# Performance work log

Hardware: AMD Instinct MI355X
Metric: run time of the kernel (lower is better)

Reference implementation:

```python
import jax, jax.numpy as jnp
import numpy as np


def setup_inputs() -> dict:
    key = jax.random.key(0)
    k1, k2, k3, k4 = jax.random.split(key, 4)
    B, T, N, D = 4, 8, 512, 256
    BT = B * T
    x = jax.random.normal(k1, (BT, N, D), dtype=jnp.float32)
    A_causal = jax.random.uniform(k2, (B, N, N), dtype=jnp.float32)
    W_qkv = jax.random.normal(k3, (3 * D, D), dtype=jnp.float32) * (D ** -0.5)
    W_proj = jax.random.normal(k4, (D, D), dtype=jnp.float32) * (D ** -0.5)
    b_proj = jnp.zeros((D,), dtype=jnp.float32)
    causal_lambda = jnp.ones((1,), dtype=jnp.float32) * 0.1
    return {
        "x": x,
        "A_causal": A_causal,
        "W_qkv": W_qkv,
        "W_proj": W_proj,
        "b_proj": b_proj,
        "causal_lambda": causal_lambda,
        "num_frames": 8,
    }


def reference(x, A_causal, W_qkv, W_proj, b_proj, causal_lambda, num_frames):
    BT, N, D = x.shape
    H = 8
    hd = D // H
    scale = hd ** -0.5
    # qkv projection (torch Linear: x @ W.T), split into q,k,v of shape [BT,H,N,hd]
    qkv = (x @ W_qkv.T).reshape(BT, N, 3, H, hd)
    qkv = jnp.transpose(qkv, (2, 0, 3, 1, 4))  # [3,BT,H,N,hd]
    q, k, v = qkv[0], qkv[1], qkv[2]
    attn = jnp.einsum("bhnd,bhmd->bhnm", q, k) * scale  # [BT,H,N,N]
    # expand A_causal [B,N,N] over frames (axis 0) and heads (broadcast axis 1)
    A_exp = jnp.repeat(A_causal, num_frames, axis=0)[:, None, :, :]  # [BT,1,N,N]
    attn = attn + causal_lambda[0] * A_exp
    attn = jax.nn.softmax(attn, axis=-1)
    out = jnp.einsum("bhnm,bhmd->bhnd", attn, v)  # [BT,H,N,hd]
    out = jnp.transpose(out, (0, 2, 1, 3)).reshape(BT, N, D)
    return out @ W_proj.T + b_proj
```

## Files before the change

### kernel.cpp

```cpp
#include <hip/hip_runtime.h>
#include <hip/hip_bf16.h>

typedef unsigned short u16;
typedef unsigned int   u32;
typedef __attribute__((ext_vector_type(8))) short short8;
typedef __attribute__((ext_vector_type(4))) float f32x4;

static __device__ __forceinline__ u16 f2b(float f) {
    __hip_bfloat16 h = __float2bfloat16(f);
    return *reinterpret_cast<u16*>(&h);
}
static __device__ __forceinline__ u32 pk2(float a, float b) {
    return (u32)f2b(a) | ((u32)f2b(b) << 16);
}

#define LDK 72

__global__ __launch_bounds__(256) void prep_A(const float* __restrict__ A,
                                              const float* __restrict__ LAM,
                                              u16* __restrict__ AB) {
    const float lam = LAM[0];
    const int i = (blockIdx.x * 256 + threadIdx.x) * 8;
    const float4 a = *(const float4*)(A + i);
    const float4 b = *(const float4*)(A + i + 4);
    uint4 o;
    o.x = pk2(lam * a.x, lam * a.y);
    o.y = pk2(lam * a.z, lam * a.w);
    o.z = pk2(lam * b.x, lam * b.y);
    o.w = pk2(lam * b.z, lam * b.w);
    *(uint4*)(AB + i) = o;
}

__global__ __launch_bounds__(256) void qkv_gemm(const float* __restrict__ X,
                                                const float* __restrict__ W,
                                                u16* __restrict__ qo,
                                                u16* __restrict__ ko,
                                                u16* __restrict__ vt) {
    __shared__ u16 SH[2 * 128 * LDK];
    u16* Xs = SH;
    u16* Ws = SH + 128 * LDK;
    const int t    = threadIdx.x;
    const int m0   = blockIdx.x << 7;
    const int o0   = blockIdx.y << 7;
    const int lane = t & 63;
    const int wid  = t >> 6;
    const int wr   = (wid >> 1) << 6;
    const int wc   = (wid & 1) << 6;
    const int ln   = lane & 15;
    const int quad = lane >> 4;

    const int r  = t >> 1;
    const int hf = (t & 1) << 5;
    const float* xg = X + (size_t)(m0 + r) * 256 + hf;
    const float* wg = W + (size_t)(o0 + r) * 256 + hf;
    uint4* xls = (uint4*)&Xs[r * LDK + hf];
    uint4* wls = (uint4*)&Ws[r * LDK + hf];

    f32x4 acc[4][4] = {};

    for (int kc = 0; kc < 256; kc += 64) {
        const float4* xp = (const float4*)(xg + kc);
        const float4* wp = (const float4*)(wg + kc);
        float xv[32], wv[32];
#pragma unroll
        for (int i = 0; i < 8; ++i) {
            float4 a = xp[i]; xv[4*i] = a.x; xv[4*i+1] = a.y; xv[4*i+2] = a.z; xv[4*i+3] = a.w;
            float4 b = wp[i]; wv[4*i] = b.x; wv[4*i+1] = b.y; wv[4*i+2] = b.z; wv[4*i+3] = b.w;
        }
        uint4 xq[4], wq[4];
#pragma unroll
        for (int i = 0; i < 4; ++i) {
            xq[i].x = pk2(xv[8*i],   xv[8*i+1]); xq[i].y = pk2(xv[8*i+2], xv[8*i+3]);
            xq[i].z = pk2(xv[8*i+4], xv[8*i+5]); xq[i].w = pk2(xv[8*i+6], xv[8*i+7]);
            wq[i].x = pk2(wv[8*i],   wv[8*i+1]); wq[i].y = pk2(wv[8*i+2], wv[8*i+3]);
            wq[i].z = pk2(wv[8*i+4], wv[8*i+5]); wq[i].w = pk2(wv[8*i+6], wv[8*i+7]);
        }
        __syncthreads();
#pragma unroll
        for (int i = 0; i < 4; ++i) { xls[i] = xq[i]; wls[i] = wq[i]; }
        __syncthreads();
#pragma unroll
        for (int kk = 0; kk < 64; kk += 32) {
            short8 a[4], b[4];
#pragma unroll
            for (int i = 0; i < 4; ++i)
                a[i] = *(const short8*)&Xs[(wr + i * 16 + ln) * LDK + kk + quad * 8];
#pragma unroll
            for (int j = 0; j < 4; ++j)
                b[j] = *(const short8*)&Ws[(wc + j * 16 + ln) * LDK + kk + quad * 8];
#pragma unroll
            for (int i = 0; i < 4; ++i)
#pragma unroll
                for (int j = 0; j < 4; ++j)
                    acc[i][j] = __builtin_amdgcn_mfma_f32_16x16x32_bf16(a[i], b[j], acc[i][j], 0, 0, 0);
        }
    }

    const int which = o0 >> 8;
    if (which < 2) {
        const float qscale = (which == 0) ? 0.17677669529663689f : 1.0f;
        u16* dst = (which == 0) ? qo : ko;
#pragma unroll
        for (int i = 0; i < 4; ++i) {
            const int mb = m0 + wr + i * 16 + quad * 4;
#pragma unroll
            for (int j = 0; j < 4; ++j) {
                const int o   = o0 + wc + j * 16 + ln;
                const int rem = o & 255;
                const int hh  = rem >> 5;
                const int dd  = rem & 31;
#pragma unroll
                for (int rr = 0; rr < 4; ++rr) {
                    const int m  = mb + rr;
                    const int bt = m >> 9;
                    const int n  = m & 511;
                    dst[(((size_t)bt * 8 + hh) * 512 + n) * 32 + dd] = f2b(acc[i][j][rr] * qscale);
                }
            }
        }
    } else {
        __syncthreads();
        u16* T = SH;
#pragma unroll
        for (int i = 0; i < 4; ++i) {
            const int ml = wr + i * 16 + quad * 4;
#pragma unroll
            for (int j = 0; j < 4; ++j) {
                const int ol = wc + j * 16 + ln;
                uint2 pv;
                pv.x = pk2(acc[i][j][0], acc[i][j][1]);
                pv.y = pk2(acc[i][j][2], acc[i][j][3]);
                *(uint2*)&T[ol * 136 + ml] = pv;
            }
        }
        __syncthreads();
        const int row = t >> 1;
        const int seg = (t & 1) << 6;
        const int o   = o0 + row;
        const int rem = o & 255;
        const int hh  = rem >> 5;
        const int dd  = rem & 31;
        const int bt  = m0 >> 9;
        u16* dstv = vt + (((size_t)bt * 8 + hh) * 32 + dd) * 512 + (m0 & 511) + seg;
#pragma unroll
        for (int kk2 = 0; kk2 < 8; ++kk2) {
            uint4 val = *(const uint4*)&T[row * 136 + seg + kk2 * 8];
            *(uint4*)(dstv + kk2 * 8) = val;
        }
    }
}

__global__ __launch_bounds__(256, 3) void attn_mfma(const u16* __restrict__ Q,
                                                    const u16* __restrict__ K,
                                                    const u16* __restrict__ VT,
                                                    const u16* __restrict__ AB,
                                                    const int* __restrict__ NF,
                                                    u16* __restrict__ AO) {
    __shared__ u16 Ks[2][128 * 40];
    __shared__ u16 Vs[2][32 * 136];
    __shared__ u16 Ps[4][32 * 40];
    const int t    = threadIdx.x;
    const int w    = t >> 6;
    const int lane = t & 63;
    const int ln   = lane & 15;
    const int quad = lane >> 4;
    const int L    = blockIdx.x;
    const int g    = (L & 7) + (((L >> 3) & 1) << 3);
    const int j    = L >> 4;
    const int qt   = g & 3;
    const int h    = j & 7;
    const int bt   = (g >> 2) * 8 + (j >> 3);
    const int bh   = bt * 8 + h;
    const int q0   = qt * 128 + w * 32;
    const size_t base = (size_t)bh * (512 * 32);
    const int b    = bt / NF[0];
    const u16* Ab  = AB + (size_t)b * 512 * 512;
    const u16* Ar0 = Ab + (size_t)(q0 + ln) * 512 + quad * 4;
    const u16* Ar1 = Ab + (size_t)(q0 + 16 + ln) * 512 + quad * 4;

    const int krow = t >> 2, kcol = (t & 3) * 8;
    const int vd   = t >> 4, vn   = (t & 15) * 8;
    const u16* Kg = K + base;
    const u16* Vg = VT + base;

    {
        uint4 s0 = *(const uint4*)(Kg + (size_t)krow * 32 + kcol);
        uint4 s1 = *(const uint4*)(Kg + (size_t)(64 + krow) * 32 + kcol);
        uint4 s2 = *(const uint4*)(Vg + (size_t)vd * 512 + vn);
        uint4 s3 = *(const uint4*)(Vg + (size_t)(16 + vd) * 512 + vn);
        *(uint4*)&Ks[0][krow * 40 + kcol]        = s0;
        *(uint4*)&Ks[0][(64 + krow) * 40 + kcol] = s1;
        *(uint4*)&Vs[0][vd * 136 + vn]           = s2;
        *(uint4*)&Vs[0][(16 + vd) * 136 + vn]    = s3;
    }

    short8 qf[2];
#pragma unroll
    for (int nt = 0; nt < 2; ++nt)
        qf[nt] = *(const short8*)(Q + base + (size_t)(q0 + nt * 16 + ln) * 32 + quad * 8);

    f32x4 o[2][2] = {};
    float lsum0 = 0.f, lsum1 = 0.f;
    __syncthreads();

    int cur = 0;
    for (int jt = 0; jt < 512; jt += 128) {
        const int nxt = cur ^ 1;
        const bool more = jt < 384;
        uint4 t0 = {}, t1 = {}, t2 = {}, t3 = {};
        if (more) {
            t0 = *(const uint4*)(Kg + (size_t)(jt + 128 + krow) * 32 + kcol);
            t1 = *(const uint4*)(Kg + (size_t)(jt + 192 + krow) * 32 + kcol);
            t2 = *(const uint4*)(Vg + (size_t)vd * 512 + jt + 128 + vn);
            t3 = *(const uint4*)(Vg + (size_t)(16 + vd) * 512 + jt + 128 + vn);
        }
        uint2 ar[16];
#pragma unroll
        for (int mt = 0; mt < 8; ++mt) {
            ar[2*mt]     = *(const uint2*)(Ar0 + jt + mt * 16);
            ar[2*mt + 1] = *(const uint2*)(Ar1 + jt + mt * 16);
        }

        float ps0 = 0.f, ps1 = 0.f;
#pragma unroll
        for (int ks = 0; ks < 4; ++ks) {
#pragma unroll
            for (int mm = 0; mm < 2; ++mm) {
                const int mt = 2 * ks + mm;
                short8 ka = *(const short8*)&Ks[cur][(mt * 16 + ln) * 40 + quad * 8];
                f32x4 c0, c1;
                c0[0] = __uint_as_float(ar[2*mt].x << 16);   c0[1] = __uint_as_float(ar[2*mt].x & 0xffff0000u);
                c0[2] = __uint_as_float(ar[2*mt].y << 16);   c0[3] = __uint_as_float(ar[2*mt].y & 0xffff0000u);
                c1[0] = __uint_as_float(ar[2*mt+1].x << 16); c1[1] = __uint_as_float(ar[2*mt+1].x & 0xffff0000u);
                c1[2] = __uint_as_float(ar[2*mt+1].y << 16); c1[3] = __uint_as_float(ar[2*mt+1].y & 0xffff0000u);
                const f32x4 s0 = __builtin_amdgcn_mfma_f32_16x16x32_bf16(ka, qf[0], c0, 0, 0, 0);
                const f32x4 s1 = __builtin_amdgcn_mfma_f32_16x16x32_bf16(ka, qf[1], c1, 0, 0, 0);
                const float p00 = __expf(s0[0]), p01 = __expf(s0[1]), p02 = __expf(s0[2]), p03 = __expf(s0[3]);
                const float p10 = __expf(s1[0]), p11 = __expf(s1[1]), p12 = __expf(s1[2]), p13 = __expf(s1[3]);
                ps0 += (p00 + p01) + (p02 + p03);
                ps1 += (p10 + p11) + (p12 + p13);
                uint2 w0; w0.x = pk2(p00, p01); w0.y = pk2(p02, p03);
                uint2 w1; w1.x = pk2(p10, p11); w1.y = pk2(p12, p13);
                *(uint2*)&Ps[w][ln * 40 + mm * 16 + quad * 4]        = w0;
                *(uint2*)&Ps[w][(16 + ln) * 40 + mm * 16 + quad * 4] = w1;
            }
            short8 pa0 = *(const short8*)&Ps[w][ln * 40 + quad * 8];
            short8 pa1 = *(const short8*)&Ps[w][(16 + ln) * 40 + quad * 8];
            short8 vb0 = *(const short8*)&Vs[cur][ln * 136 + ks * 32 + quad * 8];
            short8 vb1 = *(const short8*)&Vs[cur][(16 + ln) * 136 + ks * 32 + quad * 8];
            o[0][0] = __builtin_amdgcn_mfma_f32_16x16x32_bf16(pa0, vb0, o[0][0], 0, 0, 0);
            o[0][1] = __builtin_amdgcn_mfma_f32_16x16x32_bf16(pa0, vb1, o[0][1], 0, 0, 0);
            o[1][0] = __builtin_amdgcn_mfma_f32_16x16x32_bf16(pa1, vb0, o[1][0], 0, 0, 0);
            o[1][1] = __builtin_amdgcn_mfma_f32_16x16x32_bf16(pa1, vb1, o[1][1], 0, 0, 0);
        }

        if (more) {
            *(uint4*)&Ks[nxt][krow * 40 + kcol]        = t0;
            *(uint4*)&Ks[nxt][(64 + krow) * 40 + kcol] = t1;
            *(uint4*)&Vs[nxt][vd * 136 + vn]           = t2;
            *(uint4*)&Vs[nxt][(16 + vd) * 136 + vn]    = t3;
        }
        ps0 += __shfl_xor(ps0, 16); ps0 += __shfl_xor(ps0, 32); lsum0 += ps0;
        ps1 += __shfl_xor(ps1, 16); ps1 += __shfl_xor(ps1, 32); lsum1 += ps1;
        __syncthreads();
        cur = nxt;
    }

#pragma unroll
    for (int r = 0; r < 4; ++r) {
        const int src = quad * 4 + r;
        const float i0 = 1.f / __shfl(lsum0, src);
        const float i1 = 1.f / __shfl(lsum1, src);
        const int n0 = qt * 128 + w * 32 + quad * 4 + r;
#pragma unroll
        for (int ntd = 0; ntd < 2; ++ntd) {
            AO[((size_t)bt * 512 + n0) * 256 + h * 32 + ntd * 16 + ln]      = f2b(o[0][ntd][r] * i0);
            AO[((size_t)bt * 512 + n0 + 16) * 256 + h * 32 + ntd * 16 + ln] = f2b(o[1][ntd][r] * i1);
        }
    }
}

__global__ __launch_bounds__(256) void proj_gemm(const u16* __restrict__ X,
                                                 const float* __restrict__ W,
                                                 const float* __restrict__ BIAS,
                                                 float* __restrict__ OUT) {
    __shared__ u16 Xs[128 * LDK];
    __shared__ u16 Ws[128 * LDK];
    const int t    = threadIdx.x;
    const int m0   = blockIdx.x << 7;
    const int o0   = blockIdx.y << 7;
    const int lane = t & 63;
    const int wid  = t >> 6;
    const int wr   = (wid >> 1) << 6;
    const int wc   = (wid & 1) << 6;
    const int ln   = lane & 15;
    const int quad = lane >> 4;

    const int r  = t >> 1;
    const int hf = (t & 1) << 5;
    const u16*   xg = X + (size_t)(m0 + r) * 256 + hf;
    const float* wg = W + (size_t)(o0 + r) * 256 + hf;
    uint4* xls = (uint4*)&Xs[r * LDK + hf];
    uint4* wls = (uint4*)&Ws[r * LDK + hf];

    f32x4 acc[4][4] = {};

    for (int kc = 0; kc < 256; kc += 64) {
        const uint4*  xp = (const uint4*)(xg + kc);
        const float4* wp = (const float4*)(wg + kc);
        uint4 x0 = xp[0], x1 = xp[1], x2 = xp[2], x3 = xp[3];
        float wv[32];
#pragma unroll
        for (int i = 0; i < 8; ++i) {
            float4 b = wp[i]; wv[4*i] = b.x; wv[4*i+1] = b.y; wv[4*i+2] = b.z; wv[4*i+3] = b.w;
        }
        uint4 wq[4];
#pragma unroll
        for (int i = 0; i < 4; ++i) {
            wq[i].x = pk2(wv[8*i],   wv[8*i+1]); wq[i].y = pk2(wv[8*i+2], wv[8*i+3]);
            wq[i].z = pk2(wv[8*i+4], wv[8*i+5]); wq[i].w = pk2(wv[8*i+6], wv[8*i+7]);
        }
        __syncthreads();
        xls[0] = x0; xls[1] = x1; xls[2] = x2; xls[3] = x3;
#pragma unroll
        for (int i = 0; i < 4; ++i) wls[i] = wq[i];
        __syncthreads();
#pragma unroll
        for (int kk = 0; kk < 64; kk += 32) {
            short8 a[4], b[4];
#pragma unroll
            for (int i = 0; i < 4; ++i)
                a[i] = *(const short8*)&Xs[(wr + i * 16 + ln) * LDK + kk + quad * 8];
#pragma unroll
            for (int j = 0; j < 4; ++j)
                b[j] = *(const short8*)&Ws[(wc + j * 16 + ln) * LDK + kk + quad * 8];
#pragma unroll
            for (int i = 0; i < 4; ++i)
#pragma unroll
                for (int j = 0; j < 4; ++j)
                    acc[i][j] = __builtin_amdgcn_mfma_f32_16x16x32_bf16(a[i], b[j], acc[i][j], 0, 0, 0);
        }
    }

#pragma unroll
    for (int i = 0; i < 4; ++i) {
        const int mb = m0 + wr + i * 16 + quad * 4;
#pragma unroll
        for (int j = 0; j < 4; ++j) {
            const int o  = o0 + wc + j * 16 + ln;
            const float bo = BIAS[o];
#pragma unroll
            for (int rr = 0; rr < 4; ++rr) {
                const int m = mb + rr;
                OUT[(size_t)m * 256 + o] = acc[i][j][rr] + bo;
            }
        }
    }
}

extern "C" void kernel_launch(void* const* d_in, const int* in_sizes, int n_in,
                              void* d_out, int out_size, void* d_ws, size_t ws_size,
                              hipStream_t stream) {
    (void)in_sizes; (void)n_in; (void)out_size; (void)ws_size;
    const float* x     = (const float*)d_in[0];
    const float* A     = (const float*)d_in[1];
    const float* Wqkv  = (const float*)d_in[2];
    const float* Wproj = (const float*)d_in[3];
    const float* bproj = (const float*)d_in[4];
    const float* lam   = (const float*)d_in[5];
    const int*   nf    = (const int*)d_in[6];
    float* out = (float*)d_out;

    u16* q  = (u16*)d_ws;
    u16* k  = q + 4194304;
    u16* vt = k + 4194304;
    u16* ao = vt + 4194304;
    u16* AB = ao + 4194304;

    prep_A  <<<dim3(512), 256, 0, stream>>>(A, lam, AB);
    qkv_gemm<<<dim3(128, 6), 256, 0, stream>>>(x, Wqkv, q, k, vt);
    attn_mfma<<<dim3(1024), 256, 0, stream>>>(q, k, vt, AB, nf, ao);
    proj_gemm<<<dim3(128, 2), 256, 0, stream>>>(ao, Wproj, bproj, out);
}
```

Measured before the change: 168.1 us.

## Pre-convert weights to bf16 in prep kernel and prefetch bias tiles in attention

The prep kernel now also converts W_qkv and W_proj to bf16 once. Both GEMMs then load bf16 weights directly instead of reading fp32 and converting in every block. The attention loop prefetches the next bias tile into registers one iteration ahead and drops the conditional on the last K/V prefetch by wrapping the index. This costs extra registers and one redundant tile load at the end of each attention block.

Result: faster. 161.4 us (-4.0%).

```diff
diff --git a/kernel.cpp b/kernel.cpp
--- a/kernel.cpp
+++ b/kernel.cpp
@@ -16,23 +16,34 @@
 
 #define LDK 72
 
-__global__ __launch_bounds__(256) void prep_A(const float* __restrict__ A,
-                                              const float* __restrict__ LAM,
-                                              u16* __restrict__ AB) {
-    const float lam = LAM[0];
-    const int i = (blockIdx.x * 256 + threadIdx.x) * 8;
-    const float4 a = *(const float4*)(A + i);
-    const float4 b = *(const float4*)(A + i + 4);
+__global__ __launch_bounds__(256) void prep(const float* __restrict__ A,
+                                            const float* __restrict__ LAM,
+                                            const float* __restrict__ Wq,
+                                            const float* __restrict__ Wp,
+                                            u16* __restrict__ AB,
+                                            u16* __restrict__ wqb,
+                                            u16* __restrict__ wpb) {
+    const int bid = blockIdx.x;
+    const float* src;
+    u16* dst;
+    float scale;
+    int base;
+    if (bid < 512)      { src = A;  dst = AB;  scale = LAM[0]; base = bid * 2048; }
+    else if (bid < 608) { src = Wq; dst = wqb; scale = 1.0f;   base = (bid - 512) * 2048; }
+    else                { src = Wp; dst = wpb; scale = 1.0f;   base = (bid - 608) * 2048; }
+    const int i = base + threadIdx.x * 8;
+    const float4 a = *(const float4*)(src + i);
+    const float4 b = *(const float4*)(src + i + 4);
     uint4 o;
-    o.x = pk2(lam * a.x, lam * a.y);
-    o.y = pk2(lam * a.z, lam * a.w);
-    o.z = pk2(lam * b.x, lam * b.y);
-    o.w = pk2(lam * b.z, lam * b.w);
-    *(uint4*)(AB + i) = o;
+    o.x = pk2(scale * a.x, scale * a.y);
+    o.y = pk2(scale * a.z, scale * a.w);
+    o.z = pk2(scale * b.x, scale * b.y);
+    o.w = pk2(scale * b.z, scale * b.w);
+    *(uint4*)(dst + i) = o;
 }
 
 __global__ __launch_bounds__(256) void qkv_gemm(const float* __restrict__ X,
-                                                const float* __restrict__ W,
+                                                const u16* __restrict__ WB,
                                                 u16* __restrict__ qo,
                                                 u16* __restrict__ ko,
                                                 u16* __restrict__ vt) {
@@ -52,7 +63,7 @@
     const int r  = t >> 1;
     const int hf = (t & 1) << 5;
     const float* xg = X + (size_t)(m0 + r) * 256 + hf;
-    const float* wg = W + (size_t)(o0 + r) * 256 + hf;
+    const u16*   wg = WB + (size_t)(o0 + r) * 256 + hf;
     uint4* xls = (uint4*)&Xs[r * LDK + hf];
     uint4* wls = (uint4*)&Ws[r * LDK + hf];
 
@@ -60,24 +71,23 @@
 
     for (int kc = 0; kc < 256; kc += 64) {
         const float4* xp = (const float4*)(xg + kc);
-        const float4* wp = (const float4*)(wg + kc);
-        float xv[32], wv[32];
+        const uint4*  wp = (const uint4*)(wg + kc);
+        float xv[32];
 #pragma unroll
         for (int i = 0; i < 8; ++i) {
             float4 a = xp[i]; xv[4*i] = a.x; xv[4*i+1] = a.y; xv[4*i+2] = a.z; xv[4*i+3] = a.w;
-            float4 b = wp[i]; wv[4*i] = b.x; wv[4*i+1] = b.y; wv[4*i+2] = b.z; wv[4*i+3] = b.w;
-        }
-        uint4 xq[4], wq[4];
+        }
+        uint4 w0 = wp[0], w1 = wp[1], w2 = wp[2], w3 = wp[3];
+        uint4 xq[4];
 #pragma unroll
         for (int i = 0; i < 4; ++i) {
             xq[i].x = pk2(xv[8*i],   xv[8*i+1]); xq[i].y = pk2(xv[8*i+2], xv[8*i+3]);
             xq[i].z = pk2(xv[8*i+4], xv[8*i+5]); xq[i].w = pk2(xv[8*i+6], xv[8*i+7]);
-            wq[i].x = pk2(wv[8*i],   wv[8*i+1]); wq[i].y = pk2(wv[8*i+2], wv[8*i+3]);
-            wq[i].z = pk2(wv[8*i+4], wv[8*i+5]); wq[i].w = pk2(wv[8*i+6], wv[8*i+7]);
-        }
-        __syncthreads();
-#pragma unroll
-        for (int i = 0; i < 4; ++i) { xls[i] = xq[i]; wls[i] = wq[i]; }
+        }
+        __syncthreads();
+#pragma unroll
+        for (int i = 0; i < 4; ++i) xls[i] = xq[i];
+        wls[0] = w0; wls[1] = w1; wls[2] = w2; wls[3] = w3;
         __syncthreads();
 #pragma unroll
         for (int kk = 0; kk < 64; kk += 32) {
@@ -193,6 +203,12 @@
         *(uint4*)&Vs[0][vd * 136 + vn]           = s2;
         *(uint4*)&Vs[0][(16 + vd) * 136 + vn]    = s3;
     }
+    uint2 ar[16];
+#pragma unroll
+    for (int mt = 0; mt < 8; ++mt) {
+        ar[2*mt]     = *(const uint2*)(Ar0 + mt * 16);
+        ar[2*mt + 1] = *(const uint2*)(Ar1 + mt * 16);
+    }
 
     short8 qf[2];
 #pragma unroll
@@ -206,19 +222,16 @@
     int cur = 0;
     for (int jt = 0; jt < 512; jt += 128) {
         const int nxt = cur ^ 1;
-        const bool more = jt < 384;
-        uint4 t0 = {}, t1 = {}, t2 = {}, t3 = {};
-        if (more) {
-            t0 = *(const uint4*)(Kg + (size_t)(jt + 128 + krow) * 32 + kcol);
-            t1 = *(const uint4*)(Kg + (size_t)(jt + 192 + krow) * 32 + kcol);
-            t2 = *(const uint4*)(Vg + (size_t)vd * 512 + jt + 128 + vn);
-            t3 = *(const uint4*)(Vg + (size_t)(16 + vd) * 512 + jt + 128 + vn);
-        }
-        uint2 ar[16];
+        const int jn  = (jt + 128) & 511;
+        uint4 t0 = *(const uint4*)(Kg + (size_t)(jn + krow) * 32 + kcol);
+        uint4 t1 = *(const uint4*)(Kg + (size_t)(jn + 64 + krow) * 32 + kcol);
+        uint4 t2 = *(const uint4*)(Vg + (size_t)vd * 512 + jn + vn);
+        uint4 t3 = *(const uint4*)(Vg + (size_t)(16 + vd) * 512 + jn + vn);
+        uint2 arn[16];
 #pragma unroll
         for (int mt = 0; mt < 8; ++mt) {
-            ar[2*mt]     = *(const uint2*)(Ar0 + jt + mt * 16);
-            ar[2*mt + 1] = *(const uint2*)(Ar1 + jt + mt * 16);
+            arn[2*mt]     = *(const uint2*)(Ar0 + jn + mt * 16);
+            arn[2*mt + 1] = *(const uint2*)(Ar1 + jn + mt * 16);
         }
 
         float ps0 = 0.f, ps1 = 0.f;
@@ -254,15 +267,15 @@
             o[1][1] = __builtin_amdgcn_mfma_f32_16x16x32_bf16(pa1, vb1, o[1][1], 0, 0, 0);
         }
 
-        if (more) {
-            *(uint4*)&Ks[nxt][krow * 40 + kcol]        = t0;
-            *(uint4*)&Ks[nxt][(64 + krow) * 40 + kcol] = t1;
-            *(uint4*)&Vs[nxt][vd * 136 + vn]           = t2;
-            *(uint4*)&Vs[nxt][(16 + vd) * 136 + vn]    = t3;
-        }
+        *(uint4*)&Ks[nxt][krow * 40 + kcol]        = t0;
+        *(uint4*)&Ks[nxt][(64 + krow) * 40 + kcol] = t1;
+        *(uint4*)&Vs[nxt][vd * 136 + vn]           = t2;
+        *(uint4*)&Vs[nxt][(16 + vd) * 136 + vn]    = t3;
         ps0 += __shfl_xor(ps0, 16); ps0 += __shfl_xor(ps0, 32); lsum0 += ps0;
         ps1 += __shfl_xor(ps1, 16); ps1 += __shfl_xor(ps1, 32); lsum1 += ps1;
         __syncthreads();
+#pragma unroll
+        for (int i = 0; i < 16; ++i) ar[i] = arn[i];
         cur = nxt;
     }
 
@@ -281,7 +294,7 @@
 }
 
 __global__ __launch_bounds__(256) void proj_gemm(const u16* __restrict__ X,
-                                                 const float* __restrict__ W,
+                                                 const u16* __restrict__ WB,
                                                  const float* __restrict__ BIAS,
                                                  float* __restrict__ OUT) {
     __shared__ u16 Xs[128 * LDK];
@@ -298,32 +311,21 @@
 
     const int r  = t >> 1;
     const int hf = (t & 1) << 5;
-    const u16*   xg = X + (size_t)(m0 + r) * 256 + hf;
-    const float* wg = W + (size_t)(o0 + r) * 256 + hf;
+    const u16* xg = X + (size_t)(m0 + r) * 256 + hf;
+    const u16* wg = WB + (size_t)(o0 + r) * 256 + hf;
     uint4* xls = (uint4*)&Xs[r * LDK + hf];
     uint4* wls = (uint4*)&Ws[r * LDK + hf];
 
     f32x4 acc[4][4] = {};
 
     for (int kc = 0; kc < 256; kc += 64) {
-        const uint4*  xp = (const uint4*)(xg + kc);
-        const float4* wp = (const float4*)(wg + kc);
+        const uint4* xp = (const uint4*)(xg + kc);
+        const uint4* wp = (const uint4*)(wg + kc);
         uint4 x0 = xp[0], x1 = xp[1], x2 = xp[2], x3 = xp[3];
-        float wv[32];
-#pragma unroll
-        for (int i = 0; i < 8; ++i) {
-            float4 b = wp[i]; wv[4*i] = b.x; wv[4*i+1] = b.y; wv[4*i+2] = b.z; wv[4*i+3] = b.w;
-        }
-        uint4 wq[4];
-#pragma unroll
-        for (int i = 0; i < 4; ++i) {
-            wq[i].x = pk2(wv[8*i],   wv[8*i+1]); wq[i].y = pk2(wv[8*i+2], wv[8*i+3]);
-            wq[i].z = pk2(wv[8*i+4], wv[8*i+5]); wq[i].w = pk2(wv[8*i+6], wv[8*i+7]);
-        }
+        uint4 w0 = wp[0], w1 = wp[1], w2 = wp[2], w3 = wp[3];
         __syncthreads();
         xls[0] = x0; xls[1] = x1; xls[2] = x2; xls[3] = x3;
-#pragma unroll
-        for (int i = 0; i < 4; ++i) wls[i] = wq[i];
+        wls[0] = w0; wls[1] = w1; wls[2] = w2; wls[3] = w3;
         __syncthreads();
 #pragma unroll
         for (int kk = 0; kk < 64; kk += 32) {
@@ -371,14 +373,16 @@
     const int*   nf    = (const int*)d_in[6];
     float* out = (float*)d_out;
 
-    u16* q  = (u16*)d_ws;
-    u16* k  = q + 4194304;
-    u16* vt = k + 4194304;
-    u16* ao = vt + 4194304;
-    u16* AB = ao + 4194304;
-
-    prep_A  <<<dim3(512), 256, 0, stream>>>(A, lam, AB);
-    qkv_gemm<<<dim3(128, 6), 256, 0, stream>>>(x, Wqkv, q, k, vt);
+    u16* q   = (u16*)d_ws;
+    u16* k   = q + 4194304;
+    u16* vt  = k + 4194304;
+    u16* ao  = vt + 4194304;
+    u16* AB  = ao + 4194304;
+    u16* wqb = AB + 1048576;
+    u16* wpb = wqb + 196608;
+
+    prep    <<<dim3(640), 256, 0, stream>>>(A, lam, Wqkv, Wproj, AB, wqb, wpb);
+    qkv_gemm<<<dim3(128, 6), 256, 0, stream>>>(x, wqb, q, k, vt);
     attn_mfma<<<dim3(1024), 256, 0, stream>>>(q, k, vt, AB, nf, ao);
-    proj_gemm<<<dim3(128, 2), 256, 0, stream>>>(ao, Wproj, bproj, out);
-}
+    proj_gemm<<<dim3(128, 2), 256, 0, stream>>>(ao, wpb, bproj, out);
+}
```
